# Performance work log

Hardware: AMD Instinct MI355X
Metric: run time of the kernel (lower is better)

The kernel has to match this reference:

```python
import jax, jax.numpy as jnp
import numpy as np

GROUPS = 8
HIDDEN = 2048
T = 4096
LEAKY = 1.0
RADIUS = 100.0


def setup_inputs() -> dict:
    key = jax.random.key(0)
    k1, k2, k3 = jax.random.split(key, 3)
    x = jax.random.normal(k1, (T, 1), dtype=jnp.float32)
    W_ih = jax.random.normal(k2, (HIDDEN, 1), dtype=jnp.float32)
    # scale recurrent weights roughly like an ESN initializer would
    W_hh = jax.random.normal(k3, (GROUPS, HIDDEN, HIDDEN), dtype=jnp.float32) / jnp.sqrt(HIDDEN).astype(jnp.float32)
    return {"x": x, "W_ih": W_ih, "W_hh": W_hh}


def reference(x, W_ih, W_hh):
    # x: [T, input_size]; W_ih: [H, input_size]; W_hh: [G, H, H]
    G, H, _ = W_hh.shape
    # per-group leaky rate: leaky * (G - i) / G  (activation='default')
    lr = (LEAKY * (G - jnp.arange(G, dtype=x.dtype)) / G)[:, None]  # [G, 1]

    def step(h, x_t):
        # h: [G, H] per-group hidden states (batch of 1 flattened)
        ih = x_t @ W_ih.T                                   # [H], shared across groups
        pre = ih[None, :] + jnp.einsum('gh,gih->gi', h, W_hh)  # [G, H]
        # self_normalizing_default: (1-lr)*prev + lr*radius*pre/||pre||
        nrm = jnp.linalg.norm(pre, axis=1, keepdims=True)   # Frobenius norm per group
        h_new = (1.0 - lr) * h + lr * RADIUS * pre / nrm
        return h_new, h_new.reshape(-1)                     # concat groups -> [G*H]

    h0 = jnp.zeros((G, H), dtype=x.dtype)
    _, out = jax.lax.scan(step, h0, x)                      # out: [T, G*H]
    return out
```

## Files before the change

kernel.cpp:

```cpp
#include <hip/hip_runtime.h>
#include <math.h>

#define GROUPS   8
#define HIDDEN   2048
#define TSTEPS   4096
#define RADIUS_F 100.0f
#define BPG      32
#define NBLOCKS  (GROUPS * BPG)
#define BLOCK    512
#define ROWS_PB  64
#define ROWS_PW  8
#define GH       (GROUPS * HIDDEN)

typedef float vfloat4 __attribute__((ext_vector_type(4)));

__global__ __launch_bounds__(BLOCK, 2) void esn_persistent(
    const float* __restrict__ x,
    const float* __restrict__ W_ih,
    const float* __restrict__ W_hh,
    float* __restrict__ out,
    float* preBuf,
    unsigned* ctr)
{
    const int tid  = threadIdx.x;
    const int wave = tid >> 6;
    const int lane = tid & 63;
    const int g    = blockIdx.x & (GROUPS - 1);
    const int sub  = blockIdx.x >> 3;
    const int rowBase = sub * ROWS_PB;

    __shared__ float h_lds[HIDDEN];
    __shared__ float wih_lds[ROWS_PB];
    __shared__ float red[BLOCK / 64];

    ((float4*)h_lds)[tid] = make_float4(0.f, 0.f, 0.f, 0.f);
    if (tid < ROWS_PB / 4)
        ((float4*)wih_lds)[tid] = ((const float4*)(W_ih + rowBase))[tid];
    __syncthreads();

    const float lr  = (float)(GROUPS - g) / (float)GROUPS;
    const float olr = 1.0f - lr;
    const float lrR = lr * RADIUS_F;

    const float* Wg = W_hh + ((size_t)g * HIDDEN + rowBase) * (size_t)HIDDEN;
    unsigned* myctr = ctr + g * 64;

    for (int t = 0; t < TSTEPS; ++t) {
        const int buf = t & 1;
        float* pb = preBuf + (size_t)buf * GH + g * HIDDEN;
        const float xt = x[t];

        float acc[ROWS_PW] = {0.f, 0.f, 0.f, 0.f, 0.f, 0.f, 0.f, 0.f};
        #pragma unroll
        for (int k = 0; k < 8; ++k) {
            const float4 hv = *(const float4*)&h_lds[4 * lane + 256 * k];
            #pragma unroll
            for (int r = 0; r < ROWS_PW; ++r) {
                const float4 wv =
                    ((const float4*)(Wg + (size_t)(wave * ROWS_PW + r) * HIDDEN))[lane + 64 * k];
                acc[r] = fmaf(wv.x, hv.x, acc[r]);
                acc[r] = fmaf(wv.y, hv.y, acc[r]);
                acc[r] = fmaf(wv.z, hv.z, acc[r]);
                acc[r] = fmaf(wv.w, hv.w, acc[r]);
            }
        }
        #pragma unroll
        for (int r = 0; r < ROWS_PW; ++r) {
            float a = acc[r];
            #pragma unroll
            for (int off = 32; off; off >>= 1)
                a += __shfl_xor(a, off, 64);
            acc[r] = a;
        }
        float myv = acc[0];
        #pragma unroll
        for (int r = 1; r < ROWS_PW; ++r)
            if (lane == r) myv = acc[r];
        if (lane < ROWS_PW) {
            const int rowL = wave * ROWS_PW + lane;
            const float pre = fmaf(xt, wih_lds[rowL], myv);
            __hip_atomic_store(&pb[rowBase + rowL], pre,
                               __ATOMIC_RELAXED, __HIP_MEMORY_SCOPE_AGENT);
        }

        __syncthreads();
        if (tid == 0) {
            __hip_atomic_fetch_add(myctr, 1u, __ATOMIC_RELEASE, __HIP_MEMORY_SCOPE_AGENT);
            const unsigned tgt = (unsigned)(BPG * (t + 1));
            while (__hip_atomic_load(myctr, __ATOMIC_RELAXED, __HIP_MEMORY_SCOPE_AGENT) < tgt)
                __builtin_amdgcn_s_sleep(4);
        }
        __syncthreads();

        float* pg = preBuf + (size_t)buf * GH + g * HIDDEN;
        const float p0 = __hip_atomic_load(&pg[tid * 4 + 0], __ATOMIC_RELAXED, __HIP_MEMORY_SCOPE_AGENT);
        const float p1 = __hip_atomic_load(&pg[tid * 4 + 1], __ATOMIC_RELAXED, __HIP_MEMORY_SCOPE_AGENT);
        const float p2 = __hip_atomic_load(&pg[tid * 4 + 2], __ATOMIC_RELAXED, __HIP_MEMORY_SCOPE_AGENT);
        const float p3 = __hip_atomic_load(&pg[tid * 4 + 3], __ATOMIC_RELAXED, __HIP_MEMORY_SCOPE_AGENT);

        float ss = p0 * p0 + p1 * p1 + p2 * p2 + p3 * p3;
        #pragma unroll
        for (int off = 32; off; off >>= 1)
            ss += __shfl_xor(ss, off, 64);
        if (lane == 0) red[wave] = ss;
        __syncthreads();
        float s = 0.f;
        #pragma unroll
        for (int w = 0; w < BLOCK / 64; ++w) s += red[w];
        const float sc = lrR / sqrtf(s);

        const float4 h4 = *(const float4*)&h_lds[tid * 4];
        float4 hn;
        hn.x = olr * h4.x + sc * p0;
        hn.y = olr * h4.y + sc * p1;
        hn.z = olr * h4.z + sc * p2;
        hn.w = olr * h4.w + sc * p3;
        *(float4*)&h_lds[tid * 4] = hn;

        if (tid >= rowBase / 4 && tid < rowBase / 4 + ROWS_PB / 4) {
            vfloat4 hv4;
            hv4.x = hn.x; hv4.y = hn.y; hv4.z = hn.z; hv4.w = hn.w;
            vfloat4* op = (vfloat4*)&out[(size_t)t * GH + g * HIDDEN + tid * 4];
            __builtin_nontemporal_store(hv4, op);
        }
        __syncthreads();
    }
}

extern "C" void kernel_launch(void* const* d_in, const int* in_sizes, int n_in,
                              void* d_out, int out_size, void* d_ws, size_t ws_size,
                              hipStream_t stream) {
    const float* x   = (const float*)d_in[0];
    const float* Wih = (const float*)d_in[1];
    const float* Whh = (const float*)d_in[2];
    float* out = (float*)d_out;

    unsigned* ctr  = (unsigned*)d_ws;
    float* preBuf  = (float*)((char*)d_ws + 4096);

    (void)hipMemsetAsync(d_ws, 0, 4096, stream);

    void* args[] = { (void*)&x, (void*)&Wih, (void*)&Whh,
                     (void*)&out, (void*)&preBuf, (void*)&ctr };
    (void)hipLaunchCooperativeKernel((const void*)esn_persistent,
                                     dim3(NBLOCKS), dim3(BLOCK), args, 0, stream);
}
```

Before: 32.35 ms.

## Keep recurrent weight slice resident in registers and LDS across timesteps

```diff
diff --git a/kernel.cpp b/kernel.cpp
--- a/kernel.cpp
+++ b/kernel.cpp
@@ -9,8 +9,11 @@
 #define NBLOCKS  (GROUPS * BPG)
 #define BLOCK    512
 #define ROWS_PB  64
-#define ROWS_PW  8
 #define GH       (GROUPS * HIDDEN)
+
+#define J_REG  44
+#define J_LDS  6
+#define J_TAIL 14
 
 typedef float vfloat4 __attribute__((ext_vector_type(4)));
 
@@ -28,10 +31,24 @@
     const int g    = blockIdx.x & (GROUPS - 1);
     const int sub  = blockIdx.x >> 3;
     const int rowBase = sub * ROWS_PB;
+    const int r = tid >> 3;
+    const int c = tid & 7;
 
-    __shared__ float h_lds[HIDDEN];
-    __shared__ float wih_lds[ROWS_PB];
-    __shared__ float red[BLOCK / 64];
+    __shared__ float  h_lds[HIDDEN];
+    __shared__ float4 wlds[J_LDS * BLOCK];
+    __shared__ float  wih_lds[ROWS_PB];
+    __shared__ float  red[BLOCK / 64];
+
+    const float4* row4 =
+        (const float4*)(W_hh + ((size_t)(g * HIDDEN + rowBase + r)) * HIDDEN);
+
+    float4 wreg[J_REG];
+    #pragma unroll
+    for (int j = 0; j < J_REG; ++j)
+        wreg[j] = row4[8 * j + c];
+    #pragma unroll
+    for (int j = 0; j < J_LDS; ++j)
+        wlds[j * BLOCK + tid] = row4[8 * (J_REG + j) + c];
 
     ((float4*)h_lds)[tid] = make_float4(0.f, 0.f, 0.f, 0.f);
     if (tid < ROWS_PB / 4)
@@ -42,7 +59,10 @@
     const float olr = 1.0f - lr;
     const float lrR = lr * RADIUS_F;
 
-    const float* Wg = W_hh + ((size_t)g * HIDDEN + rowBase) * (size_t)HIDDEN;
+    const float4* tail4 = row4 + 8 * (J_REG + J_LDS) + c;
+    const float4* h4c   = (const float4*)h_lds + c;
+    const float4* wl4   = wlds + tid;
+
     unsigned* myctr = ctr + g * 64;
 
     for (int t = 0; t < TSTEPS; ++t) {
@@ -50,36 +70,55 @@
         float* pb = preBuf + (size_t)buf * GH + g * HIDDEN;
         const float xt = x[t];
 
-        float acc[ROWS_PW] = {0.f, 0.f, 0.f, 0.f, 0.f, 0.f, 0.f, 0.f};
+        float acc = 0.f;
+
+        float4 ta[7], tb[7];
         #pragma unroll
-        for (int k = 0; k < 8; ++k) {
-            const float4 hv = *(const float4*)&h_lds[4 * lane + 256 * k];
-            #pragma unroll
-            for (int r = 0; r < ROWS_PW; ++r) {
-                const float4 wv =
-                    ((const float4*)(Wg + (size_t)(wave * ROWS_PW + r) * HIDDEN))[lane + 64 * k];
-                acc[r] = fmaf(wv.x, hv.x, acc[r]);
-                acc[r] = fmaf(wv.y, hv.y, acc[r]);
-                acc[r] = fmaf(wv.z, hv.z, acc[r]);
-                acc[r] = fmaf(wv.w, hv.w, acc[r]);
-            }
+        for (int j = 0; j < 7; ++j) ta[j] = tail4[8 * j];
+
+        #pragma unroll
+        for (int j = 0; j < J_REG; ++j) {
+            const float4 hv = h4c[8 * j];
+            acc = fmaf(wreg[j].x, hv.x, acc);
+            acc = fmaf(wreg[j].y, hv.y, acc);
+            acc = fmaf(wreg[j].z, hv.z, acc);
+            acc = fmaf(wreg[j].w, hv.w, acc);
         }
         #pragma unroll
-        for (int r = 0; r < ROWS_PW; ++r) {
-            float a = acc[r];
-            #pragma unroll
-            for (int off = 32; off; off >>= 1)
-                a += __shfl_xor(a, off, 64);
-            acc[r] = a;
+        for (int j = 0; j < J_LDS; ++j) {
+            const float4 wv = wl4[j * BLOCK];
+            const float4 hv = h4c[8 * (J_REG + j)];
+            acc = fmaf(wv.x, hv.x, acc);
+            acc = fmaf(wv.y, hv.y, acc);
+            acc = fmaf(wv.z, hv.z, acc);
+            acc = fmaf(wv.w, hv.w, acc);
         }
-        float myv = acc[0];
+        __builtin_amdgcn_sched_barrier(0);
         #pragma unroll
-        for (int r = 1; r < ROWS_PW; ++r)
-            if (lane == r) myv = acc[r];
-        if (lane < ROWS_PW) {
-            const int rowL = wave * ROWS_PW + lane;
-            const float pre = fmaf(xt, wih_lds[rowL], myv);
-            __hip_atomic_store(&pb[rowBase + rowL], pre,
+        for (int j = 0; j < 7; ++j) tb[j] = tail4[8 * (7 + j)];
+        #pragma unroll
+        for (int j = 0; j < 7; ++j) {
+            const float4 hv = h4c[8 * (J_REG + J_LDS + j)];
+            acc = fmaf(ta[j].x, hv.x, acc);
+            acc = fmaf(ta[j].y, hv.y, acc);
+            acc = fmaf(ta[j].z, hv.z, acc);
+            acc = fmaf(ta[j].w, hv.w, acc);
+        }
+        #pragma unroll
+        for (int j = 0; j < 7; ++j) {
+            const float4 hv = h4c[8 * (J_REG + J_LDS + 7 + j)];
+            acc = fmaf(tb[j].x, hv.x, acc);
+            acc = fmaf(tb[j].y, hv.y, acc);
+            acc = fmaf(tb[j].z, hv.z, acc);
+            acc = fmaf(tb[j].w, hv.w, acc);
+        }
+
+        acc += __shfl_xor(acc, 1, 64);
+        acc += __shfl_xor(acc, 2, 64);
+        acc += __shfl_xor(acc, 4, 64);
+        if (c == 0) {
+            const float pre = fmaf(xt, wih_lds[r], acc);
+            __hip_atomic_store(&pb[rowBase + r], pre,
                                __ATOMIC_RELAXED, __HIP_MEMORY_SCOPE_AGENT);
         }
 
@@ -88,7 +127,7 @@
             __hip_atomic_fetch_add(myctr, 1u, __ATOMIC_RELEASE, __HIP_MEMORY_SCOPE_AGENT);
             const unsigned tgt = (unsigned)(BPG * (t + 1));
             while (__hip_atomic_load(myctr, __ATOMIC_RELAXED, __HIP_MEMORY_SCOPE_AGENT) < tgt)
-                __builtin_amdgcn_s_sleep(4);
+                __builtin_amdgcn_s_sleep(2);
         }
         __syncthreads();
 
```

Result: faster. 27.86 ms (-13.9%).
